# Kernel tuning notes

Measured on AMD Instinct MI355X. Metric: run time of the kernel, lower is better.

The kernel has to match this reference:

```python
import jax, jax.numpy as jnp
import numpy as np
from jax import lax

F1, D, F2 = 8, 2, 16
CTX = 64           # context = 1.0 s * 64 Hz
NCH = 64           # EEG channels
POOL1, POOL2 = 2, 5
BN_EPS = 1e-5


def _conv2d(x, w, b, padding, groups=1):
    y = lax.conv_general_dilated(x, w, (1, 1), padding,
                                 dimension_numbers=('NCHW', 'OIHW', 'NCHW'),
                                 feature_group_count=groups)
    return y + b[None, :, None, None]


def _bn(x, g, b, m, v):
    scale = g / jnp.sqrt(v + BN_EPS)
    return (x - m[None, :, None, None]) * scale[None, :, None, None] + b[None, :, None, None]


def _avgpool_w(x, k):
    y = lax.reduce_window(x, jnp.float32(0), lax.add, (1, 1, 1, k), (1, 1, 1, k), 'VALID')
    return y / k


def setup_inputs() -> dict:
    key = jax.random.key(0)
    ks = jax.random.split(key, 24)
    B, C, eegL = 16, NCH, 256
    f32 = jnp.float32
    inp = {
        'eeg': jax.random.normal(ks[0], (B, C, eegL), f32),
        'env': jax.random.normal(ks[1], (B, 2, eegL), f32),
        # conv1: Conv2d(1, F1, (1,3), padding='same')
        'conv1_w': jax.random.normal(ks[2], (F1, 1, 1, 3), f32) * 0.3,
        'conv1_b': jax.random.normal(ks[3], (F1,), f32) * 0.05,
        'bn1_g': jax.random.uniform(ks[4], (F1,), f32, 0.8, 1.2),
        'bn1_b': jax.random.normal(ks[5], (F1,), f32) * 0.05,
        'bn1_m': jax.random.normal(ks[6], (F1,), f32) * 0.1,
        'bn1_v': jax.random.uniform(ks[7], (F1,), f32, 0.5, 1.5),
        # conv2: Conv2d(F1, F1*D, (NCH,1), 'valid', groups=F1)
        'conv2_w': jax.random.normal(ks[8], (F1 * D, 1, NCH, 1), f32) * 0.05,
        'conv2_b': jax.random.normal(ks[9], (F1 * D,), f32) * 0.05,
        'bn2_g': jax.random.uniform(ks[10], (F1 * D,), f32, 0.8, 1.2),
        'bn2_b': jax.random.normal(ks[11], (F1 * D,), f32) * 0.05,
        'bn2_m': jax.random.normal(ks[12], (F1 * D,), f32) * 0.1,
        'bn2_v': jax.random.uniform(ks[13], (F1 * D,), f32, 0.5, 1.5),
        # conv3: depthwise Conv2d(F1*D, F1*D, (1,3), 'same', groups=F1*D)
        'conv3_w': jax.random.normal(ks[14], (F1 * D, 1, 1, 3), f32) * 0.3,
        'conv3_b': jax.random.normal(ks[15], (F1 * D,), f32) * 0.05,
        # conv4: pointwise Conv2d(F1*D, F2, (1,1))
        'conv4_w': jax.random.normal(ks[16], (F2, F1 * D, 1, 1), f32) * 0.2,
        'conv4_b': jax.random.normal(ks[17], (F2,), f32) * 0.05,
        'bn3_g': jax.random.uniform(ks[18], (F2,), f32, 0.8, 1.2),
        'bn3_b': jax.random.normal(ks[19], (F2,), f32) * 0.05,
        'bn3_m': jax.random.normal(ks[20], (F2,), f32) * 0.1,
        'bn3_v': jax.random.uniform(ks[21], (F2,), f32, 0.5, 1.5),
        # linear: F2 * (CTX // (POOL1*POOL2)) -> 1
        'lin_w': jax.random.normal(ks[22], (1, F2 * (CTX // (POOL1 * POOL2))), f32) * 0.1,
        'lin_b': jax.random.normal(ks[23], (1,), f32) * 0.05,
    }
    return inp


def _forward(eeg, conv1_w, conv1_b, bn1_g, bn1_b, bn1_m, bn1_v,
             conv2_w, conv2_b, bn2_g, bn2_b, bn2_m, bn2_v,
             conv3_w, conv3_b, conv4_w, conv4_b,
             bn3_g, bn3_b, bn3_m, bn3_v, lin_w, lin_b):
    B, C, eegL = eeg.shape
    L = eegL - CTX + 1
    # extract all overlapping windows: [B, C, L, CTX] -> [B*L, 1, C, CTX]
    idx = jnp.arange(L)[:, None] + jnp.arange(CTX)[None, :]
    win = eeg[:, :, idx]                      # [B, C, L, CTX]
    x = win.transpose(0, 2, 1, 3).reshape(B * L, 1, C, CTX)
    x = _conv2d(x, conv1_w, conv1_b, ((0, 0), (1, 1)))            # same pad on time
    x = _bn(x, bn1_g, bn1_b, bn1_m, bn1_v)
    x = _conv2d(x, conv2_w, conv2_b, ((0, 0), (0, 0)), groups=F1)  # spatial conv -> H=1
    x = _bn(x, bn2_g, bn2_b, bn2_m, bn2_v)
    x = jax.nn.elu(x)
    x = _avgpool_w(x, POOL1)
    x = _conv2d(x, conv3_w, conv3_b, ((0, 0), (1, 1)), groups=F1 * D)  # depthwise temporal
    x = _conv2d(x, conv4_w, conv4_b, ((0, 0), (0, 0)))                 # pointwise
    x = _bn(x, bn3_g, bn3_b, bn3_m, bn3_v)
    x = jax.nn.elu(x)
    x = _avgpool_w(x, POOL2)
    x = x.reshape(B * L, -1)                  # [B*L, F2*6]
    y = x @ lin_w.T + lin_b                   # [B*L, 1]
    return y.reshape(B, L)


def reference(eeg, env, conv1_w, conv1_b, bn1_g, bn1_b, bn1_m, bn1_v,
              conv2_w, conv2_b, bn2_g, bn2_b, bn2_m, bn2_v,
              conv3_w, conv3_b, conv4_w, conv4_b,
              bn3_g, bn3_b, bn3_m, bn3_v, lin_w, lin_b):
    assert env.shape[1] == 2  # n_streams check (env unused by the math)
    return _forward(eeg, conv1_w, conv1_b, bn1_g, bn1_b, bn1_m, bn1_v,
                    conv2_w, conv2_b, bn2_g, bn2_b, bn2_m, bn2_v,
                    conv3_w, conv3_b, conv4_w, conv4_b,
                    bn3_g, bn3_b, bn3_m, bn3_v, lin_w, lin_b)
```

## Files before the change

### kernel.cpp

```cpp
#include <hip/hip_runtime.h>
#include <math.h>

#define BN_EPS 1e-5f
#define LWIN   193
#define WPB    16
#define NBL    13
#define SLOC   96
#define STR    97

typedef __attribute__((address_space(1))) const unsigned int gl_u32;
typedef __attribute__((address_space(3))) unsigned int lds_u32;

__device__ __forceinline__ float elu(float x) { return x > 0.f ? x : expm1f(x); }

__global__ __launch_bounds__(256) void eegnet_fused(
    const float* __restrict__ eeg,
    const float* __restrict__ c1w, const float* __restrict__ c1b,
    const float* __restrict__ bn1g, const float* __restrict__ bn1b,
    const float* __restrict__ bn1m, const float* __restrict__ bn1v,
    const float* __restrict__ w2,  const float* __restrict__ c2b,
    const float* __restrict__ bn2g, const float* __restrict__ bn2b,
    const float* __restrict__ bn2m, const float* __restrict__ bn2v,
    const float* __restrict__ c3w, const float* __restrict__ c3b,
    const float* __restrict__ c4w, const float* __restrict__ c4b,
    const float* __restrict__ bn3g, const float* __restrict__ bn3b,
    const float* __restrict__ bn3m, const float* __restrict__ bn3v,
    const float* __restrict__ linw, const float* __restrict__ linb,
    float* __restrict__ out)
{
    const int b   = blockIdx.x;
    const int L0  = blockIdx.y * WPB;
    const int g0  = L0 - 3;
    const int tid = threadIdx.x;
    const int lane16 = tid & 15;
    const int grp16  = tid >> 4;

    __shared__ __align__(16) float Eg[64 * SLOC];
    __shared__ float4 w2t4[64 * 4];
    __shared__ float  Ul[16][STR];
    __shared__ float  El[16][STR];
    __shared__ float  P2[16][STR];
    __shared__ float  Ql[16][STR];
    __shared__ float  Ef[16][STR];
    __shared__ float  S5[16][STR];
    __shared__ float  cs[512];
    __shared__ float  q0s[16][17], q1s[16][17];

    const float* ebase = eeg + b * 64 * 256;

    {
        const int wv = tid >> 6, ln = tid & 63;
        #pragma unroll
        for (int j = 0; j < 6; ++j) {
            const int n    = wv * 6 + j;
            const int fidx = n * 256 + ln * 4;
            const int c    = fidx / SLOC;
            const int i    = fidx - c * SLOC;
            const int s    = g0 + i;
            if (s >= 0 && s <= 252) {
                __builtin_amdgcn_global_load_lds((gl_u32*)(ebase + c * 256 + s),
                                                 (lds_u32*)&Eg[n * 256], 16, 0, 0);
            } else {
                const float* row = ebase + c * 256;
                const int e0 = s     < 0 ? 0 : (s     > 255 ? 255 : s);
                const int e1 = s + 1 < 0 ? 0 : (s + 1 > 255 ? 255 : s + 1);
                const int e2 = s + 2 < 0 ? 0 : (s + 2 > 255 ? 255 : s + 2);
                const int e3 = s + 3 < 0 ? 0 : (s + 3 > 255 ? 255 : s + 3);
                *reinterpret_cast<float4*>(&Eg[fidx]) =
                    make_float4(row[e0], row[e1], row[e2], row[e3]);
            }
        }
    }

    {
        const int og = tid >> 6, c = tid & 63, o0 = og * 4;
        w2t4[c * 4 + og] = make_float4(w2[(o0    ) * 64 + c], w2[(o0 + 1) * 64 + c],
                                       w2[(o0 + 2) * 64 + c], w2[(o0 + 3) * 64 + c]);
    }

    if (tid < 64) {
        const int f = tid & 15, q = tid >> 4;
        float s2p = 0.f;
        #pragma unroll
        for (int k = 0; k < 16; ++k) s2p += w2[f * 64 + q * 16 + k];
        s2p += __shfl_xor(s2p, 16);
        s2p += __shfl_xor(s2p, 32);
        if (tid < 16) {
            const int g = f >> 1;
            const float s1 = bn1g[g] / sqrtf(bn1v[g] + BN_EPS);
            const float o1 = bn1b[g] - bn1m[g] * s1;
            const float s2 = bn2g[f] / sqrtf(bn2v[f] + BN_EPS);
            const float o2 = bn2b[f] - bn2m[f] * s2;
            const float ss = s2 * s1;
            cs[      f] = ss * c1w[g * 3 + 0];
            cs[ 16 + f] = ss * c1w[g * 3 + 1];
            cs[ 32 + f] = ss * c1w[g * 3 + 2];
            cs[ 48 + f] = s2 * (fmaf(s1, c1b[g], o1) * s2p + c2b[f]) + o2;
            cs[ 64 + f] = c3w[f * 3 + 0];
            cs[ 80 + f] = c3w[f * 3 + 1];
            cs[ 96 + f] = c3w[f * 3 + 2];
            cs[112 + f] = c3b[f];
        }
    } else if (tid < 128) {
        const int j = tid - 64, f = j & 15, quad = j >> 4;
        const float s3 = bn3g[f] / sqrtf(bn3v[f] + BN_EPS);
        if (quad == 0)
            cs[128 + f] = fmaf(s3, c4b[f], bn3b[f] - bn3m[f] * s3);
        #pragma unroll
        for (int k = 0; k < 4; ++k) {
            const int o = quad * 4 + k;
            cs[144 + o * 16 + f] = s3 * c4w[f * 16 + o];
        }
    } else if (tid < 224) {
        cs[400 + tid - 128] = linw[tid - 128];
    } else if (tid == 224) {
        cs[496] = linb[0];
    }
    __syncthreads();

    {
        const int p  = tid & 63;
        const int og = tid >> 6;
        const bool two = (p < 32);
        float a0 = 0.f, a1 = 0.f, a2 = 0.f, a3 = 0.f;
        float b0 = 0.f, b1 = 0.f, b2 = 0.f, b3 = 0.f;
        #pragma unroll 8
        for (int c = 0; c < 64; ++c) {
            const float4 w = w2t4[c * 4 + og];
            const float  e = Eg[c * SLOC + p];
            a0 = fmaf(w.x, e, a0); a1 = fmaf(w.y, e, a1);
            a2 = fmaf(w.z, e, a2); a3 = fmaf(w.w, e, a3);
            if (two) {
                const float e2 = Eg[c * SLOC + p + 64];
                b0 = fmaf(w.x, e2, b0); b1 = fmaf(w.y, e2, b1);
                b2 = fmaf(w.z, e2, b2); b3 = fmaf(w.w, e2, b3);
            }
        }
        const int o0 = og * 4;
        Ul[o0    ][p] = a0; Ul[o0 + 1][p] = a1;
        Ul[o0 + 2][p] = a2; Ul[o0 + 3][p] = a3;
        if (two) {
            Ul[o0    ][p + 64] = b0; Ul[o0 + 1][p + 64] = b1;
            Ul[o0 + 2][p + 64] = b2; Ul[o0 + 3][p + 64] = b3;
        }
    }
    __syncthreads();

    #pragma unroll
    for (int k = 0; k < 6; ++k) {
        const int i = grp16 + 16 * k, sg = g0 + i, o = lane16;
        const float um = (sg >= 1)   ? Ul[o][i > 0 ? i - 1 : 0] : 0.f;
        const float uc = Ul[o][i];
        const float up = (sg <= 254) ? Ul[o][i < SLOC - 1 ? i + 1 : SLOC - 1] : 0.f;
        El[o][i] = elu(fmaf(cs[o], um, fmaf(cs[16 + o], uc, fmaf(cs[32 + o], up, cs[48 + o]))));
    }
    __syncthreads();

    #pragma unroll
    for (int k = 0; k < 6; ++k) {
        const int i = grp16 + 16 * k, o = lane16;
        const int ip = i < SLOC - 1 ? i + 1 : SLOC - 1;
        P2[o][i] = 0.5f * (El[o][i] + El[o][ip]);
    }
    __syncthreads();

    #pragma unroll
    for (int k = 0; k < 6; ++k) {
        const int i = grp16 + 16 * k, o = lane16;
        const int im = i >= 2 ? i - 2 : 0;
        const int ip = i < SLOC - 2 ? i + 2 : SLOC - 1;
        Ql[o][i] = fmaf(cs[64 + o], P2[o][im],
                   fmaf(cs[80 + o], P2[o][i],
                   fmaf(cs[96 + o], P2[o][ip], cs[112 + o])));
    }
    __syncthreads();

    #pragma unroll
    for (int k = 0; k < 6; ++k) {
        const int i = grp16 + 16 * k, f = lane16;
        float r = cs[128 + f];
        #pragma unroll
        for (int o = 0; o < 16; ++o)
            r = fmaf(cs[144 + o * 16 + f], Ql[o][i], r);
        Ef[f][i] = elu(r);
    }
    __syncthreads();

    #pragma unroll
    for (int k = 0; k < 6; ++k) {
        const int i = grp16 + 16 * k, f = lane16;
        const int i2 = i + 2 < SLOC ? i + 2 : SLOC - 1;
        const int i4 = i + 4 < SLOC ? i + 4 : SLOC - 1;
        const int i6 = i + 6 < SLOC ? i + 6 : SLOC - 1;
        const int i8 = i + 8 < SLOC ? i + 8 : SLOC - 1;
        S5[f][i] = Ef[f][i] + Ef[f][i2] + Ef[f][i4] + Ef[f][i6] + Ef[f][i8];
    }
    __syncthreads();

    {
        const int w = grp16, o = lane16, l = L0 + w;
        if (l < LWIN) {
            const int li = w + 3;
            const float z0 = fmaf(cs[16 + o], Ul[o][li], fmaf(cs[32 + o], Ul[o][li + 1], cs[48 + o]));
            const float P0 = 0.5f * (elu(z0) + El[o][li + 1]);
            const float pa = P2[o][li + 2], pb = P2[o][li + 4];
            q0s[w][o] = fmaf(cs[80 + o], P0, fmaf(cs[96 + o], pa, cs[112 + o]));
            q1s[w][o] = fmaf(cs[64 + o], P0, fmaf(cs[80 + o], pa, fmaf(cs[96 + o], pb, cs[112 + o])));
        }
    }
    __syncthreads();

    {
        const int w = grp16, f = lane16, l = L0 + w;
        float part = 0.f;
        if (l < LWIN) {
            const int li = w + 3;
            float r0 = cs[128 + f], r1 = r0;
            #pragma unroll
            for (int o = 0; o < 16; ++o) {
                const float wt = cs[144 + o * 16 + f];
                r0 = fmaf(wt, q0s[w][o], r0);
                r1 = fmaf(wt, q1s[w][o], r1);
            }
            part = cs[400 + f * 6] * (elu(r0) + elu(r1) - Ef[f][li] - Ef[f][li + 2]);
            #pragma unroll
            for (int g = 0; g < 6; ++g)
                part = fmaf(cs[400 + f * 6 + g], S5[f][li + 10 * g], part);
        }
        part += __shfl_xor(part, 1);
        part += __shfl_xor(part, 2);
        part += __shfl_xor(part, 4);
        part += __shfl_xor(part, 8);
        if (f == 0 && l < LWIN) out[b * LWIN + l] = fmaf(0.2f, part, cs[496]);
    }
}

extern "C" void kernel_launch(void* const* d_in, const int* in_sizes, int n_in,
                              void* d_out, int out_size, void* d_ws, size_t ws_size,
                              hipStream_t stream) {
    const float* eeg  = (const float*)d_in[0];
    const float* c1w  = (const float*)d_in[2];
    const float* c1b  = (const float*)d_in[3];
    const float* bn1g = (const float*)d_in[4];
    const float* bn1b = (const float*)d_in[5];
    const float* bn1m = (const float*)d_in[6];
    const float* bn1v = (const float*)d_in[7];
    const float* w2   = (const float*)d_in[8];
    const float* c2b  = (const float*)d_in[9];
    const float* bn2g = (const float*)d_in[10];
    const float* bn2b = (const float*)d_in[11];
    const float* bn2m = (const float*)d_in[12];
    const float* bn2v = (const float*)d_in[13];
    const float* c3w  = (const float*)d_in[14];
    const float* c3b  = (const float*)d_in[15];
    const float* c4w  = (const float*)d_in[16];
    const float* c4b  = (const float*)d_in[17];
    const float* bn3g = (const float*)d_in[18];
    const float* bn3b = (const float*)d_in[19];
    const float* bn3m = (const float*)d_in[20];
    const float* bn3v = (const float*)d_in[21];
    const float* linw = (const float*)d_in[22];
    const float* linb = (const float*)d_in[23];

    eegnet_fused<<<dim3(16, NBL), 256, 0, stream>>>(
        eeg, c1w, c1b, bn1g, bn1b, bn1m, bn1v, w2, c2b,
        bn2g, bn2b, bn2m, bn2v, c3w, c3b, c4w, c4b,
        bn3g, bn3b, bn3m, bn3v, linw, linb, (float*)d_out);
}
```

Measured before the change: 15.58 us.

## Read EEG and spatial weights directly from global memory instead of LDS staging

Removes the async global-to-LDS staging of the EEG window and the transposed w2 table. The spatial conv now reads EEG samples and weights straight from global memory, with weight addresses made wave-uniform through readfirstlane so they can become scalar loads. The first block barrier is dropped as well. This saves LDS traffic, LDS capacity and one sync, but each thread now issues per-channel global loads whose latency can only be hidden by the cache. Clamped indices replace the old edge handling, and out-of-range positions appear to be masked later anyway.

```diff
diff --git a/kernel.cpp b/kernel.cpp
--- a/kernel.cpp
+++ b/kernel.cpp
@@ -7,9 +7,6 @@
 #define NBL    13
 #define SLOC   96
 #define STR    97
-
-typedef __attribute__((address_space(1))) const unsigned int gl_u32;
-typedef __attribute__((address_space(3))) unsigned int lds_u32;
 
 __device__ __forceinline__ float elu(float x) { return x > 0.f ? x : expm1f(x); }
 
@@ -35,48 +32,12 @@
     const int lane16 = tid & 15;
     const int grp16  = tid >> 4;
 
-    __shared__ __align__(16) float Eg[64 * SLOC];
-    __shared__ float4 w2t4[64 * 4];
-    __shared__ float  Ul[16][STR];
-    __shared__ float  El[16][STR];
-    __shared__ float  P2[16][STR];
-    __shared__ float  Ql[16][STR];
-    __shared__ float  Ef[16][STR];
-    __shared__ float  S5[16][STR];
-    __shared__ float  cs[512];
-    __shared__ float  q0s[16][17], q1s[16][17];
+    __shared__ float Ul[16][STR], El[16][STR], P2[16][STR], Ql[16][STR];
+    __shared__ float Ef[16][STR], S5[16][STR];
+    __shared__ float cs[512];
+    __shared__ float q0s[16][17], q1s[16][17];
 
     const float* ebase = eeg + b * 64 * 256;
-
-    {
-        const int wv = tid >> 6, ln = tid & 63;
-        #pragma unroll
-        for (int j = 0; j < 6; ++j) {
-            const int n    = wv * 6 + j;
-            const int fidx = n * 256 + ln * 4;
-            const int c    = fidx / SLOC;
-            const int i    = fidx - c * SLOC;
-            const int s    = g0 + i;
-            if (s >= 0 && s <= 252) {
-                __builtin_amdgcn_global_load_lds((gl_u32*)(ebase + c * 256 + s),
-                                                 (lds_u32*)&Eg[n * 256], 16, 0, 0);
-            } else {
-                const float* row = ebase + c * 256;
-                const int e0 = s     < 0 ? 0 : (s     > 255 ? 255 : s);
-                const int e1 = s + 1 < 0 ? 0 : (s + 1 > 255 ? 255 : s + 1);
-                const int e2 = s + 2 < 0 ? 0 : (s + 2 > 255 ? 255 : s + 2);
-                const int e3 = s + 3 < 0 ? 0 : (s + 3 > 255 ? 255 : s + 3);
-                *reinterpret_cast<float4*>(&Eg[fidx]) =
-                    make_float4(row[e0], row[e1], row[e2], row[e3]);
-            }
-        }
-    }
-
-    {
-        const int og = tid >> 6, c = tid & 63, o0 = og * 4;
-        w2t4[c * 4 + og] = make_float4(w2[(o0    ) * 64 + c], w2[(o0 + 1) * 64 + c],
-                                       w2[(o0 + 2) * 64 + c], w2[(o0 + 3) * 64 + c]);
-    }
 
     if (tid < 64) {
         const int f = tid & 15, q = tid >> 4;
@@ -116,27 +77,32 @@
     } else if (tid == 224) {
         cs[496] = linb[0];
     }
-    __syncthreads();
 
     {
         const int p  = tid & 63;
-        const int og = tid >> 6;
+        const int og = __builtin_amdgcn_readfirstlane(tid >> 6);
+        const int o0 = og * 4;
+        const float* wr0 = w2 + (o0    ) * 64;
+        const float* wr1 = w2 + (o0 + 1) * 64;
+        const float* wr2 = w2 + (o0 + 2) * 64;
+        const float* wr3 = w2 + (o0 + 3) * 64;
+        int s1 = g0 + p;       s1 = s1 < 0 ? 0 : (s1 > 255 ? 255 : s1);
+        int s2 = g0 + p + 64;  s2 = s2 < 0 ? 0 : (s2 > 255 ? 255 : s2);
         const bool two = (p < 32);
         float a0 = 0.f, a1 = 0.f, a2 = 0.f, a3 = 0.f;
         float b0 = 0.f, b1 = 0.f, b2 = 0.f, b3 = 0.f;
         #pragma unroll 8
         for (int c = 0; c < 64; ++c) {
-            const float4 w = w2t4[c * 4 + og];
-            const float  e = Eg[c * SLOC + p];
-            a0 = fmaf(w.x, e, a0); a1 = fmaf(w.y, e, a1);
-            a2 = fmaf(w.z, e, a2); a3 = fmaf(w.w, e, a3);
+            const float e   = ebase[c * 256 + s1];
+            const float w0c = wr0[c], w1c = wr1[c], w2c = wr2[c], w3c = wr3[c];
+            a0 = fmaf(w0c, e, a0); a1 = fmaf(w1c, e, a1);
+            a2 = fmaf(w2c, e, a2); a3 = fmaf(w3c, e, a3);
             if (two) {
-                const float e2 = Eg[c * SLOC + p + 64];
-                b0 = fmaf(w.x, e2, b0); b1 = fmaf(w.y, e2, b1);
-                b2 = fmaf(w.z, e2, b2); b3 = fmaf(w.w, e2, b3);
+                const float e2 = ebase[c * 256 + s2];
+                b0 = fmaf(w0c, e2, b0); b1 = fmaf(w1c, e2, b1);
+                b2 = fmaf(w2c, e2, b2); b3 = fmaf(w3c, e2, b3);
             }
         }
-        const int o0 = og * 4;
         Ul[o0    ][p] = a0; Ul[o0 + 1][p] = a1;
         Ul[o0 + 2][p] = a2; Ul[o0 + 3][p] = a3;
         if (two) {
```

Result: slower. 19.35 us (+24.2%).

## Remap per-stage work so each wave owns channels, removing block barriers

Applied to the files above, without the earlier changes.

Each wave now processes four whole channels across all positions through the spatial conv, ELU, pooling and depthwise stages. Because the data stays within one wave, most __syncthreads between stages are removed. The pointwise conv is also register-blocked over four output channels with float4 weight loads. The stages still depend on each other through LDS inside a wave, so correctness relies on wave-level execution order, and the new mapping changes the LDS access patterns.

```diff
diff --git a/kernel.cpp b/kernel.cpp
--- a/kernel.cpp
+++ b/kernel.cpp
@@ -28,32 +28,30 @@
     const float* __restrict__ linw, const float* __restrict__ linb,
     float* __restrict__ out)
 {
-    const int b   = blockIdx.x;
-    const int L0  = blockIdx.y * WPB;
-    const int g0  = L0 - 3;
-    const int tid = threadIdx.x;
+    const int b    = blockIdx.x;
+    const int L0   = blockIdx.y * WPB;
+    const int g0   = L0 - 3;
+    const int tid  = threadIdx.x;
+    const int lane = tid & 63;
+    const int og   = tid >> 6;
+    const int o0   = og * 4;
     const int lane16 = tid & 15;
     const int grp16  = tid >> 4;
 
     __shared__ __align__(16) float Eg[64 * SLOC];
     __shared__ float4 w2t4[64 * 4];
-    __shared__ float  Ul[16][STR];
-    __shared__ float  El[16][STR];
-    __shared__ float  P2[16][STR];
-    __shared__ float  Ql[16][STR];
-    __shared__ float  Ef[16][STR];
-    __shared__ float  S5[16][STR];
-    __shared__ float  cs[512];
+    __shared__ float  Ul[16][STR], El[16][STR], P2[16][STR], Ql[16][STR];
+    __shared__ float  Ef[16][STR], S5[16][STR];
+    __shared__ __align__(16) float cs[512];
     __shared__ float  q0s[16][17], q1s[16][17];
 
     const float* ebase = eeg + b * 64 * 256;
 
     {
-        const int wv = tid >> 6, ln = tid & 63;
         #pragma unroll
         for (int j = 0; j < 6; ++j) {
-            const int n    = wv * 6 + j;
-            const int fidx = n * 256 + ln * 4;
+            const int n    = og * 6 + j;
+            const int fidx = n * 256 + lane * 4;
             const int c    = fidx / SLOC;
             const int i    = fidx - c * SLOC;
             const int s    = g0 + i;
@@ -73,7 +71,7 @@
     }
 
     {
-        const int og = tid >> 6, c = tid & 63, o0 = og * 4;
+        const int c = lane;
         w2t4[c * 4 + og] = make_float4(w2[(o0    ) * 64 + c], w2[(o0 + 1) * 64 + c],
                                        w2[(o0 + 2) * 64 + c], w2[(o0 + 3) * 64 + c]);
     }
@@ -119,8 +117,7 @@
     __syncthreads();
 
     {
-        const int p  = tid & 63;
-        const int og = tid >> 6;
+        const int p = lane;
         const bool two = (p < 32);
         float a0 = 0.f, a1 = 0.f, a2 = 0.f, a3 = 0.f;
         float b0 = 0.f, b1 = 0.f, b2 = 0.f, b3 = 0.f;
@@ -136,7 +133,6 @@
                 b2 = fmaf(w.z, e2, b2); b3 = fmaf(w.w, e2, b3);
             }
         }
-        const int o0 = og * 4;
         Ul[o0    ][p] = a0; Ul[o0 + 1][p] = a1;
         Ul[o0 + 2][p] = a2; Ul[o0 + 3][p] = a3;
         if (two) {
@@ -144,58 +140,93 @@
             Ul[o0 + 2][p + 64] = b2; Ul[o0 + 3][p + 64] = b3;
         }
     }
+
+    #pragma unroll
+    for (int j = 0; j < 4; ++j) {
+        const int o = o0 + j;
+        #pragma unroll
+        for (int h = 0; h < 2; ++h) {
+            const int i = lane + 64 * h;
+            if (h == 0 || lane < 32) {
+                const int sg = g0 + i;
+                const float um = (sg >= 1)   ? Ul[o][i > 0 ? i - 1 : 0] : 0.f;
+                const float uc = Ul[o][i];
+                const float up = (sg <= 254) ? Ul[o][i < SLOC - 1 ? i + 1 : SLOC - 1] : 0.f;
+                El[o][i] = elu(fmaf(cs[o], um, fmaf(cs[16 + o], uc, fmaf(cs[32 + o], up, cs[48 + o]))));
+            }
+        }
+    }
+
+    #pragma unroll
+    for (int j = 0; j < 4; ++j) {
+        const int o = o0 + j;
+        #pragma unroll
+        for (int h = 0; h < 2; ++h) {
+            const int i = lane + 64 * h;
+            if (h == 0 || lane < 32) {
+                const int ip = i < SLOC - 1 ? i + 1 : SLOC - 1;
+                P2[o][i] = 0.5f * (El[o][i] + El[o][ip]);
+            }
+        }
+    }
+
+    #pragma unroll
+    for (int j = 0; j < 4; ++j) {
+        const int o = o0 + j;
+        #pragma unroll
+        for (int h = 0; h < 2; ++h) {
+            const int i = lane + 64 * h;
+            if (h == 0 || lane < 32) {
+                const int im = i >= 2 ? i - 2 : 0;
+                const int ip = i < SLOC - 2 ? i + 2 : SLOC - 1;
+                Ql[o][i] = fmaf(cs[64 + o], P2[o][im],
+                           fmaf(cs[80 + o], P2[o][i],
+                           fmaf(cs[96 + o], P2[o][ip], cs[112 + o])));
+            }
+        }
+    }
     __syncthreads();
 
+    {
+        const float4 k4 = *reinterpret_cast<const float4*>(&cs[128 + o0]);
+        float ra0 = k4.x, ra1 = k4.y, ra2 = k4.z, ra3 = k4.w;
+        float rb0 = k4.x, rb1 = k4.y, rb2 = k4.z, rb3 = k4.w;
+        const bool two = (lane < 32);
+        #pragma unroll
+        for (int o = 0; o < 16; ++o) {
+            const float4 w = *reinterpret_cast<const float4*>(&cs[144 + o * 16 + o0]);
+            const float qa = Ql[o][lane];
+            ra0 = fmaf(w.x, qa, ra0); ra1 = fmaf(w.y, qa, ra1);
+            ra2 = fmaf(w.z, qa, ra2); ra3 = fmaf(w.w, qa, ra3);
+            if (two) {
+                const float qb = Ql[o][lane + 64];
+                rb0 = fmaf(w.x, qb, rb0); rb1 = fmaf(w.y, qb, rb1);
+                rb2 = fmaf(w.z, qb, rb2); rb3 = fmaf(w.w, qb, rb3);
+            }
+        }
+        Ef[o0    ][lane] = elu(ra0); Ef[o0 + 1][lane] = elu(ra1);
+        Ef[o0 + 2][lane] = elu(ra2); Ef[o0 + 3][lane] = elu(ra3);
+        if (two) {
+            Ef[o0    ][lane + 64] = elu(rb0); Ef[o0 + 1][lane + 64] = elu(rb1);
+            Ef[o0 + 2][lane + 64] = elu(rb2); Ef[o0 + 3][lane + 64] = elu(rb3);
+        }
+    }
+
     #pragma unroll
-    for (int k = 0; k < 6; ++k) {
-        const int i = grp16 + 16 * k, sg = g0 + i, o = lane16;
-        const float um = (sg >= 1)   ? Ul[o][i > 0 ? i - 1 : 0] : 0.f;
-        const float uc = Ul[o][i];
-        const float up = (sg <= 254) ? Ul[o][i < SLOC - 1 ? i + 1 : SLOC - 1] : 0.f;
-        El[o][i] = elu(fmaf(cs[o], um, fmaf(cs[16 + o], uc, fmaf(cs[32 + o], up, cs[48 + o]))));
-    }
-    __syncthreads();
-
-    #pragma unroll
-    for (int k = 0; k < 6; ++k) {
-        const int i = grp16 + 16 * k, o = lane16;
-        const int ip = i < SLOC - 1 ? i + 1 : SLOC - 1;
-        P2[o][i] = 0.5f * (El[o][i] + El[o][ip]);
-    }
-    __syncthreads();
-
-    #pragma unroll
-    for (int k = 0; k < 6; ++k) {
-        const int i = grp16 + 16 * k, o = lane16;
-        const int im = i >= 2 ? i - 2 : 0;
-        const int ip = i < SLOC - 2 ? i + 2 : SLOC - 1;
-        Ql[o][i] = fmaf(cs[64 + o], P2[o][im],
-                   fmaf(cs[80 + o], P2[o][i],
-                   fmaf(cs[96 + o], P2[o][ip], cs[112 + o])));
-    }
-    __syncthreads();
-
-    #pragma unroll
-    for (int k = 0; k < 6; ++k) {
-        const int i = grp16 + 16 * k, f = lane16;
-        float r = cs[128 + f];
-        #pragma unroll
-        for (int o = 0; o < 16; ++o)
-            r = fmaf(cs[144 + o * 16 + f], Ql[o][i], r);
-        Ef[f][i] = elu(r);
-    }
-    __syncthreads();
-
-    #pragma unroll
-    for (int k = 0; k < 6; ++k) {
-        const int i = grp16 + 16 * k, f = lane16;
-        const int i2 = i + 2 < SLOC ? i + 2 : SLOC - 1;
-        const int i4 = i + 4 < SLOC ? i + 4 : SLOC - 1;
-        const int i6 = i + 6 < SLOC ? i + 6 : SLOC - 1;
-        const int i8 = i + 8 < SLOC ? i + 8 : SLOC - 1;
-        S5[f][i] = Ef[f][i] + Ef[f][i2] + Ef[f][i4] + Ef[f][i6] + Ef[f][i8];
-    }
-    __syncthreads();
+    for (int j = 0; j < 4; ++j) {
+        const int f = o0 + j;
+        #pragma unroll
+        for (int h = 0; h < 2; ++h) {
+            const int i = lane + 64 * h;
+            if (h == 0 || lane < 32) {
+                const int i2 = i + 2 < SLOC ? i + 2 : SLOC - 1;
+                const int i4 = i + 4 < SLOC ? i + 4 : SLOC - 1;
+                const int i6 = i + 6 < SLOC ? i + 6 : SLOC - 1;
+                const int i8 = i + 8 < SLOC ? i + 8 : SLOC - 1;
+                S5[f][i] = Ef[f][i] + Ef[f][i2] + Ef[f][i4] + Ef[f][i6] + Ef[f][i8];
+            }
+        }
+    }
 
     {
         const int w = grp16, o = lane16, l = L0 + w;
```

New measurement: 16.40 us. +5.2%, slower.
